# Performance work log

Measured on AMD Instinct MI355X. Metric: run time of the kernel, lower is better.

Reference implementation:

```python
import jax, jax.numpy as jnp
import numpy as np

NEG = -1e30  # finite stand-in for -inf; exp underflows to 0 in fp32, grads stay finite


def setup_inputs() -> dict:
    key = jax.random.key(0)
    k1, k2, k3 = jax.random.split(key, 3)
    B, N, M = 64, 1024, 1024
    m = jax.random.normal(k1, (B, N, M), dtype=jnp.float32)
    nrows = jax.random.randint(k2, (B,), 0, N, dtype=jnp.int64) if jax.config.read('jax_enable_x64') else jax.random.randint(k2, (B,), 0, N, dtype=jnp.int32)
    ncols = jax.random.randint(k3, (B,), 0, M, dtype=jnp.int32)
    nrows = nrows.astype(jnp.int32)
    return {"m": m, "nrows": nrows, "ncols": ncols}


def reference(m, nrows, ncols):
    max_iter, tau = 20, 1.0
    B, N, M = m.shape  # N <= M -> no-transpose branch of the original
    row_valid = jnp.arange(N)[None, :, None] < nrows[:, None, None]  # [B,N,1]
    col_valid = jnp.arange(M)[None, None, :] < ncols[:, None, None]  # [B,1,M]
    valid = row_valid & col_valid                                    # [B,N,M]

    log_m = jnp.where(valid, m / tau, NEG)

    def step(lm, _):
        # even iteration: normalize rows (sum over columns)
        lse_r = jax.scipy.special.logsumexp(lm, axis=2, keepdims=True)  # [B,N,1]
        lm = jnp.where(valid, lm - lse_r, NEG)
        # odd iteration: normalize columns (sum over rows)
        lse_c = jax.scipy.special.logsumexp(lm, axis=1, keepdims=True)  # [B,1,M]
        lm = jnp.where(valid, lm - lse_c, NEG)
        return lm, None

    log_m, _ = jax.lax.scan(step, log_m, None, length=max_iter // 2)
    return jnp.where(valid, jnp.exp(log_m), 0.0)
```

## Files before the change

### kernel.cpp

```cpp
#include <hip/hip_runtime.h>
#include <math.h>


#define BIGNEG (-1e30f)
typedef _Float16 h16;
struct alignas(16) h8 { h16 h[8]; };

#define NN 1024
#define MM 1024
#define NBLK 16

__device__ __forceinline__ float wave_max64(float v) {
#pragma unroll
    for (int o = 32; o > 0; o >>= 1) v = fmaxf(v, __shfl_xor(v, o, 64));
    return v;
}
__device__ __forceinline__ float wave_sum64(float v) {
#pragma unroll
    for (int o = 32; o > 0; o >>= 1) v += __shfl_xor(v, o, 64);
    return v;
}

__device__ __forceinline__ float ld_coh(const float* p) {
    return __hip_atomic_load(p, __ATOMIC_RELAXED, __HIP_MEMORY_SCOPE_AGENT);
}
__device__ __forceinline__ void st_coh(float* p, float v) {
    __hip_atomic_store(p, v, __ATOMIC_RELAXED, __HIP_MEMORY_SCOPE_AGENT);
}

__global__ void zero_bar(unsigned* bar, int n) {
    const int i = blockIdx.x * blockDim.x + threadIdx.x;
    if (i < n) bar[i] = 0;
}

#define BATCH_BAR()                                                            \
    do {                                                                       \
        asm volatile("s_waitcnt vmcnt(0)" ::: "memory");                       \
        __syncthreads();                                                       \
        ++phase;                                                               \
        if (threadIdx.x == 0) {                                                \
            __hip_atomic_fetch_add(ctr, 1u, __ATOMIC_RELAXED,                  \
                                   __HIP_MEMORY_SCOPE_AGENT);                  \
            while (__hip_atomic_load(ctr, __ATOMIC_RELAXED,                    \
                                     __HIP_MEMORY_SCOPE_AGENT) <               \
                   (unsigned)(phase * NBLK))                                   \
                __builtin_amdgcn_s_sleep(8);                                   \
        }                                                                      \
        __syncthreads();                                                       \
        asm volatile("" ::: "memory");                                         \
    } while (0)

__device__ __forceinline__ void reduce16(float* z, float* cs, float& uout) {
    float mx = z[0];
#pragma unroll
    for (int e = 1; e < 16; ++e) mx = fmaxf(mx, z[e]);
    mx = wave_max64(mx);
    float s = 0.f;
#pragma unroll
    for (int e = 0; e < 16; ++e) { z[e] = __expf(z[e] - mx); s += z[e]; }
    s = wave_sum64(s);
    const float rs = __builtin_amdgcn_rcpf(s);
#pragma unroll
    for (int e = 0; e < 16; ++e) cs[e] += z[e] * rs;
    uout = -(mx + __logf(s));
}

__global__ __launch_bounds__(256, 4) void sinkhorn_fused(
    const float* __restrict__ m, const int* __restrict__ nrows,
    const int* __restrict__ ncols, float* __restrict__ P,
    h16* __restrict__ mh, unsigned* __restrict__ bar, float* __restrict__ out,
    int B) {
    const int sub = blockIdx.x & (NBLK - 1);
    const int b = blockIdx.x >> 4;
    const int w = threadIdx.x >> 6;
    const int lane = threadIdx.x & 63;
    const int wid = sub * 4 + w;
    const int tid = threadIdx.x;
    const int nr = nrows[b];
    const int nc = ncols[b];
    unsigned* ctr = bar + (size_t)b * 16;
    int phase = 0;

    __shared__ float pbuf[4][64][17];
    __shared__ float vloc[MM];
    __shared__ float uloc[NN];

    const size_t mbo = (size_t)b * NN * MM;
    const size_t Psz = (size_t)B * NBLK * MM;
    float* Pw0 = P + (size_t)b * NBLK * MM + (size_t)sub * MM;
    const float* Pr0 = P + (size_t)b * NBLK * MM;

    float cs[16];
#pragma unroll
    for (int e = 0; e < 16; ++e) cs[e] = 0.f;

    if (nc > 0) {
        float mk[16];
#pragma unroll
        for (int e = 0; e < 16; ++e) {
            const int col = lane * 8 + (e >> 3) * 512 + (e & 7);
            mk[e] = (col < nc) ? 0.f : BIGNEG;
        }
        int row = wid;
        float4 A0, A1, A2, A3;
        if (row < nr) {
            const float* rp = m + mbo + (size_t)row * MM + lane * 8;
            A0 = *reinterpret_cast<const float4*>(rp);
            A1 = *reinterpret_cast<const float4*>(rp + 4);
            A2 = *reinterpret_cast<const float4*>(rp + 512);
            A3 = *reinterpret_cast<const float4*>(rp + 516);
        }
        while (row < nr) {
            const int nx = row + 64;
            float4 N0, N1, N2, N3;
            if (nx < nr) {
                const float* rq = m + mbo + (size_t)nx * MM + lane * 8;
                N0 = *reinterpret_cast<const float4*>(rq);
                N1 = *reinterpret_cast<const float4*>(rq + 4);
                N2 = *reinterpret_cast<const float4*>(rq + 512);
                N3 = *reinterpret_cast<const float4*>(rq + 516);
            }
            float z[16];
            *reinterpret_cast<float4*>(&z[0]) = A0;
            *reinterpret_cast<float4*>(&z[4]) = A1;
            *reinterpret_cast<float4*>(&z[8]) = A2;
            *reinterpret_cast<float4*>(&z[12]) = A3;
            h8 hv0, hv1;
#pragma unroll
            for (int e = 0; e < 8; ++e) hv0.h[e] = (h16)z[e];
#pragma unroll
            for (int e = 0; e < 8; ++e) hv1.h[e] = (h16)z[8 + e];
            h16* rh = mh + mbo + (size_t)row * MM + lane * 8;
            *reinterpret_cast<h8*>(rh) = hv0;
            *reinterpret_cast<h8*>(rh + 512) = hv1;
#pragma unroll
            for (int e = 0; e < 16; ++e) z[e] += mk[e];
            float u;
            reduce16(z, cs, u);
            if (lane == 0) uloc[row] = u;
            A0 = N0; A1 = N1; A2 = N2; A3 = N3;
            row = nx;
        }
    } else {
        if (lane == 0)
            for (int row = wid; row < nr; row += 64) uloc[row] = 0.f;
    }

    for (int t = 1; t <= 10; ++t) {
#pragma unroll
        for (int e = 0; e < 16; ++e) pbuf[w][lane][e] = cs[e];
        __syncthreads();
        {
            float* Pw = Pw0 + (size_t)(t & 1) * Psz;
#pragma unroll
            for (int q = 0; q < 4; ++q) {
                const int col = tid + q * 256;
                const int ls = (col >> 3) & 63;
                const int ei = ((col >> 9) << 3) | (col & 7);
                const float sum = pbuf[0][ls][ei] + pbuf[1][ls][ei] +
                                  pbuf[2][ls][ei] + pbuf[3][ls][ei];
                st_coh(Pw + col, sum);
            }
        }

        BATCH_BAR();

        {
            const float* Pr = Pr0 + (size_t)(t & 1) * Psz;
#pragma unroll
            for (int q = 0; q < 4; ++q) {
                const int col = tid + q * 256;
                float CS = 0.f;
#pragma unroll
                for (int s16 = 0; s16 < NBLK; ++s16)
                    CS += ld_coh(Pr + s16 * MM + col);
                const float vp = (t == 1) ? 0.f : vloc[col];
                const float vn = vp - __logf(CS);
                vloc[col] = fminf(fmaxf(vn, BIGNEG), 1e30f);
            }
        }
        __syncthreads();
        if (t == 10) break;

        float vvm[16];
        {
            float tmp[16];
            *reinterpret_cast<float4*>(&tmp[0]) =
                *reinterpret_cast<const float4*>(&vloc[lane * 8]);
            *reinterpret_cast<float4*>(&tmp[4]) =
                *reinterpret_cast<const float4*>(&vloc[lane * 8 + 4]);
            *reinterpret_cast<float4*>(&tmp[8]) =
                *reinterpret_cast<const float4*>(&vloc[lane * 8 + 512]);
            *reinterpret_cast<float4*>(&tmp[12]) =
                *reinterpret_cast<const float4*>(&vloc[lane * 8 + 516]);
#pragma unroll
            for (int e = 0; e < 16; ++e) {
                const int col = lane * 8 + (e >> 3) * 512 + (e & 7);
                vvm[e] = (col < nc) ? tmp[e] : BIGNEG;
            }
        }
#pragma unroll
        for (int e = 0; e < 16; ++e) cs[e] = 0.f;
        if (nc > 0) {
            int row = wid;
            while (row + 64 < nr) {
                const h16* r0 = mh + mbo + (size_t)row * MM + lane * 8;
                const h16* r1 = r0 + (size_t)64 * MM;
                const h8 a0 = *reinterpret_cast<const h8*>(r0);
                const h8 a1 = *reinterpret_cast<const h8*>(r0 + 512);
                const h8 b0 = *reinterpret_cast<const h8*>(r1);
                const h8 b1 = *reinterpret_cast<const h8*>(r1 + 512);
                float z0[16], z1[16];
#pragma unroll
                for (int e = 0; e < 8; ++e) {
                    z0[e] = (float)a0.h[e] + vvm[e];
                    z0[8 + e] = (float)a1.h[e] + vvm[8 + e];
                    z1[e] = (float)b0.h[e] + vvm[e];
                    z1[8 + e] = (float)b1.h[e] + vvm[8 + e];
                }
                float u0, u1;
                reduce16(z0, cs, u0);
                reduce16(z1, cs, u1);
                if (lane == 0) { uloc[row] = u0; uloc[row + 64] = u1; }
                row += 128;
            }
            if (row < nr) {
                const h16* r0 = mh + mbo + (size_t)row * MM + lane * 8;
                const h8 a0 = *reinterpret_cast<const h8*>(r0);
                const h8 a1 = *reinterpret_cast<const h8*>(r0 + 512);
                float z0[16];
#pragma unroll
                for (int e = 0; e < 8; ++e) {
                    z0[e] = (float)a0.h[e] + vvm[e];
                    z0[8 + e] = (float)a1.h[e] + vvm[8 + e];
                }
                float u0;
                reduce16(z0, cs, u0);
                if (lane == 0) uloc[row] = u0;
            }
        }
    }

    {
        float vvm[16];
        float tmp[16];
        *reinterpret_cast<float4*>(&tmp[0]) =
            *reinterpret_cast<const float4*>(&vloc[lane * 8]);
        *reinterpret_cast<float4*>(&tmp[4]) =
            *reinterpret_cast<const float4*>(&vloc[lane * 8 + 4]);
        *reinterpret_cast<float4*>(&tmp[8]) =
            *reinterpret_cast<const float4*>(&vloc[lane * 8 + 512]);
        *reinterpret_cast<float4*>(&tmp[12]) =
            *reinterpret_cast<const float4*>(&vloc[lane * 8 + 516]);
#pragma unroll
        for (int e = 0; e < 16; ++e) {
            const int col = lane * 8 + (e >> 3) * 512 + (e & 7);
            vvm[e] = (col < nc) ? tmp[e] : BIGNEG;
        }
        const float4 z4 = make_float4(0.f, 0.f, 0.f, 0.f);
        for (int row = wid; row < NN; row += 64) {
            float* orow = out + mbo + (size_t)row * MM + lane * 8;
            if (row < nr) {
                const float ui = uloc[row];
                const h16* rh = mh + mbo + (size_t)row * MM + lane * 8;
                const h8 h0 = *reinterpret_cast<const h8*>(rh);
                const h8 h1 = *reinterpret_cast<const h8*>(rh + 512);
                float r[16];
#pragma unroll
                for (int e = 0; e < 8; ++e) {
                    r[e] = __expf((float)h0.h[e] + ui + vvm[e]);
                    r[8 + e] = __expf((float)h1.h[e] + ui + vvm[8 + e]);
                }
                *reinterpret_cast<float4*>(orow) =
                    *reinterpret_cast<float4*>(&r[0]);
                *reinterpret_cast<float4*>(orow + 4) =
                    *reinterpret_cast<float4*>(&r[4]);
                *reinterpret_cast<float4*>(orow + 512) =
                    *reinterpret_cast<float4*>(&r[8]);
                *reinterpret_cast<float4*>(orow + 516) =
                    *reinterpret_cast<float4*>(&r[12]);
            } else {
                *reinterpret_cast<float4*>(orow) = z4;
                *reinterpret_cast<float4*>(orow + 4) = z4;
                *reinterpret_cast<float4*>(orow + 512) = z4;
                *reinterpret_cast<float4*>(orow + 516) = z4;
            }
        }
    }
}

extern "C" void kernel_launch(void* const* d_in, const int* in_sizes, int n_in,
                              void* d_out, int out_size, void* d_ws,
                              size_t ws_size, hipStream_t stream) {
    const float* m = (const float*)d_in[0];
    const int* nrows = (const int*)d_in[1];
    const int* ncols = (const int*)d_in[2];
    const int B = in_sizes[1];

    char* ws = (char*)d_ws;
    unsigned* bar = (unsigned*)ws;
    float* P = (float*)(ws + (1u << 20));
    h16* mh = (h16*)(ws + (16u << 20));
    float* out = (float*)d_out;

    const int nbar = B * 16;
    zero_bar<<<dim3((nbar + 255) / 256), dim3(256), 0, stream>>>(bar, nbar);

    sinkhorn_fused<<<dim3(B * NBLK), dim3(256), 0, stream>>>(
        m, nrows, ncols, P, mh, bar, out, B);
}
```

Before: 600.2 us.

## Work in log2 domain, drop max-subtraction, early-exit empty batches, zero-fill early

```diff
diff --git a/kernel.cpp b/kernel.cpp
--- a/kernel.cpp
+++ b/kernel.cpp
@@ -3,6 +3,7 @@
 
 
 #define BIGNEG (-1e30f)
+#define LOG2E 1.44269504f
 typedef _Float16 h16;
 struct alignas(16) h8 { h16 h[8]; };
 
@@ -10,11 +11,6 @@
 #define MM 1024
 #define NBLK 16
 
-__device__ __forceinline__ float wave_max64(float v) {
-#pragma unroll
-    for (int o = 32; o > 0; o >>= 1) v = fmaxf(v, __shfl_xor(v, o, 64));
-    return v;
-}
 __device__ __forceinline__ float wave_sum64(float v) {
 #pragma unroll
     for (int o = 32; o > 0; o >>= 1) v += __shfl_xor(v, o, 64);
@@ -50,19 +46,18 @@
         asm volatile("" ::: "memory");                                         \
     } while (0)
 
-__device__ __forceinline__ void reduce16(float* z, float* cs, float& uout) {
-    float mx = z[0];
-#pragma unroll
-    for (int e = 1; e < 16; ++e) mx = fmaxf(mx, z[e]);
-    mx = wave_max64(mx);
-    float s = 0.f;
-#pragma unroll
-    for (int e = 0; e < 16; ++e) { z[e] = __expf(z[e] - mx); s += z[e]; }
+__device__ __forceinline__ void sum16(const float* z, float* cs, float& u2) {
+    float p[16], s = 0.f;
+#pragma unroll
+    for (int e = 0; e < 16; ++e) {
+        p[e] = __builtin_amdgcn_exp2f(z[e]);
+        s += p[e];
+    }
     s = wave_sum64(s);
     const float rs = __builtin_amdgcn_rcpf(s);
 #pragma unroll
-    for (int e = 0; e < 16; ++e) cs[e] += z[e] * rs;
-    uout = -(mx + __logf(s));
+    for (int e = 0; e < 16; ++e) cs[e] += p[e] * rs;
+    u2 = -__builtin_amdgcn_logf(s);
 }
 
 __global__ __launch_bounds__(256, 4) void sinkhorn_fused(
@@ -86,6 +81,19 @@
     __shared__ float uloc[NN];
 
     const size_t mbo = (size_t)b * NN * MM;
+    const float4 z4 = make_float4(0.f, 0.f, 0.f, 0.f);
+
+    if (nr == 0 || nc == 0) {
+        for (int row = wid; row < NN; row += 64) {
+            float* orow = out + mbo + (size_t)row * MM + lane * 8;
+            *reinterpret_cast<float4*>(orow) = z4;
+            *reinterpret_cast<float4*>(orow + 4) = z4;
+            *reinterpret_cast<float4*>(orow + 512) = z4;
+            *reinterpret_cast<float4*>(orow + 516) = z4;
+        }
+        return;
+    }
+
     const size_t Psz = (size_t)B * NBLK * MM;
     float* Pw0 = P + (size_t)b * NBLK * MM + (size_t)sub * MM;
     const float* Pr0 = P + (size_t)b * NBLK * MM;
@@ -94,7 +102,7 @@
 #pragma unroll
     for (int e = 0; e < 16; ++e) cs[e] = 0.f;
 
-    if (nc > 0) {
+    {
         float mk[16];
 #pragma unroll
         for (int e = 0; e < 16; ++e) {
@@ -120,30 +128,38 @@
                 N2 = *reinterpret_cast<const float4*>(rq + 512);
                 N3 = *reinterpret_cast<const float4*>(rq + 516);
             }
-            float z[16];
-            *reinterpret_cast<float4*>(&z[0]) = A0;
-            *reinterpret_cast<float4*>(&z[4]) = A1;
-            *reinterpret_cast<float4*>(&z[8]) = A2;
-            *reinterpret_cast<float4*>(&z[12]) = A3;
+            float zs[16], zr[16];
+            *reinterpret_cast<float4*>(&zs[0]) = A0;
+            *reinterpret_cast<float4*>(&zs[4]) = A1;
+            *reinterpret_cast<float4*>(&zs[8]) = A2;
+            *reinterpret_cast<float4*>(&zs[12]) = A3;
+#pragma unroll
+            for (int e = 0; e < 16; ++e) {
+                zs[e] *= LOG2E;
+                zr[e] = zs[e] + mk[e];
+            }
             h8 hv0, hv1;
 #pragma unroll
-            for (int e = 0; e < 8; ++e) hv0.h[e] = (h16)z[e];
-#pragma unroll
-            for (int e = 0; e < 8; ++e) hv1.h[e] = (h16)z[8 + e];
+            for (int e = 0; e < 8; ++e) hv0.h[e] = (h16)zs[e];
+#pragma unroll
+            for (int e = 0; e < 8; ++e) hv1.h[e] = (h16)zs[8 + e];
             h16* rh = mh + mbo + (size_t)row * MM + lane * 8;
             *reinterpret_cast<h8*>(rh) = hv0;
             *reinterpret_cast<h8*>(rh + 512) = hv1;
-#pragma unroll
-            for (int e = 0; e < 16; ++e) z[e] += mk[e];
             float u;
-            reduce16(z, cs, u);
+            sum16(zr, cs, u);
             if (lane == 0) uloc[row] = u;
             A0 = N0; A1 = N1; A2 = N2; A3 = N3;
             row = nx;
         }
-    } else {
-        if (lane == 0)
-            for (int row = wid; row < nr; row += 64) uloc[row] = 0.f;
+    }
+
+    for (int row = nr + wid; row < NN; row += 64) {
+        float* orow = out + mbo + (size_t)row * MM + lane * 8;
+        *reinterpret_cast<float4*>(orow) = z4;
+        *reinterpret_cast<float4*>(orow + 4) = z4;
+        *reinterpret_cast<float4*>(orow + 512) = z4;
+        *reinterpret_cast<float4*>(orow + 516) = z4;
     }
 
     for (int t = 1; t <= 10; ++t) {
@@ -175,7 +191,7 @@
                 for (int s16 = 0; s16 < NBLK; ++s16)
                     CS += ld_coh(Pr + s16 * MM + col);
                 const float vp = (t == 1) ? 0.f : vloc[col];
-                const float vn = vp - __logf(CS);
+                const float vn = vp - __log2f(CS);
                 vloc[col] = fminf(fmaxf(vn, BIGNEG), 1e30f);
             }
         }
@@ -201,7 +217,7 @@
         }
 #pragma unroll
         for (int e = 0; e < 16; ++e) cs[e] = 0.f;
-        if (nc > 0) {
+        {
             int row = wid;
             while (row + 64 < nr) {
                 const h16* r0 = mh + mbo + (size_t)row * MM + lane * 8;
@@ -219,8 +235,8 @@
                     z1[8 + e] = (float)b1.h[e] + vvm[8 + e];
                 }
                 float u0, u1;
-                reduce16(z0, cs, u0);
-                reduce16(z1, cs, u1);
+                sum16(z0, cs, u0);
+                sum16(z1, cs, u1);
                 if (lane == 0) { uloc[row] = u0; uloc[row + 64] = u1; }
                 row += 128;
             }
@@ -235,7 +251,7 @@
                     z0[8 + e] = (float)a1.h[e] + vvm[8 + e];
                 }
                 float u0;
-                reduce16(z0, cs, u0);
+                sum16(z0, cs, u0);
                 if (lane == 0) uloc[row] = u0;
             }
         }
@@ -257,34 +273,26 @@
             const int col = lane * 8 + (e >> 3) * 512 + (e & 7);
             vvm[e] = (col < nc) ? tmp[e] : BIGNEG;
         }
-        const float4 z4 = make_float4(0.f, 0.f, 0.f, 0.f);
-        for (int row = wid; row < NN; row += 64) {
+        for (int row = wid; row < nr; row += 64) {
             float* orow = out + mbo + (size_t)row * MM + lane * 8;
-            if (row < nr) {
-                const float ui = uloc[row];
-                const h16* rh = mh + mbo + (size_t)row * MM + lane * 8;
-                const h8 h0 = *reinterpret_cast<const h8*>(rh);
-                const h8 h1 = *reinterpret_cast<const h8*>(rh + 512);
-                float r[16];
-#pragma unroll
-                for (int e = 0; e < 8; ++e) {
-                    r[e] = __expf((float)h0.h[e] + ui + vvm[e]);
-                    r[8 + e] = __expf((float)h1.h[e] + ui + vvm[8 + e]);
-                }
-                *reinterpret_cast<float4*>(orow) =
-                    *reinterpret_cast<float4*>(&r[0]);
-                *reinterpret_cast<float4*>(orow + 4) =
-                    *reinterpret_cast<float4*>(&r[4]);
-                *reinterpret_cast<float4*>(orow + 512) =
-                    *reinterpret_cast<float4*>(&r[8]);
-                *reinterpret_cast<float4*>(orow + 516) =
-                    *reinterpret_cast<float4*>(&r[12]);
-            } else {
-                *reinterpret_cast<float4*>(orow) = z4;
-                *reinterpret_cast<float4*>(orow + 4) = z4;
-                *reinterpret_cast<float4*>(orow + 512) = z4;
-                *reinterpret_cast<float4*>(orow + 516) = z4;
-            }
+            const float ui = uloc[row];
+            const h16* rh = mh + mbo + (size_t)row * MM + lane * 8;
+            const h8 h0 = *reinterpret_cast<const h8*>(rh);
+            const h8 h1 = *reinterpret_cast<const h8*>(rh + 512);
+            float r[16];
+#pragma unroll
+            for (int e = 0; e < 8; ++e) {
+                r[e] = __builtin_amdgcn_exp2f((float)h0.h[e] + ui + vvm[e]);
+                r[8 + e] =
+                    __builtin_amdgcn_exp2f((float)h1.h[e] + ui + vvm[8 + e]);
+            }
+            *reinterpret_cast<float4*>(orow) = *reinterpret_cast<float4*>(&r[0]);
+            *reinterpret_cast<float4*>(orow + 4) =
+                *reinterpret_cast<float4*>(&r[4]);
+            *reinterpret_cast<float4*>(orow + 512) =
+                *reinterpret_cast<float4*>(&r[8]);
+            *reinterpret_cast<float4*>(orow + 516) =
+                *reinterpret_cast<float4*>(&r[12]);
         }
     }
 }
```

Result: slower. 616.0 us (+2.6%).
